# Kernel optimization log

Measured on AMD Instinct MI355X. Metric: run time of the kernel, lower is better.

The kernel has to match this reference:

```python
import jax, jax.numpy as jnp
import numpy as np

NUM_GROUPS = 100
GROUP_SIZE = 100  # uniform group sizes -> total_rows = 10000
TOTAL_ROWS = NUM_GROUPS * GROUP_SIZE
NUM_CLASSES = 1000
BATCH = 4096
EPS = 1e-12


def setup_inputs() -> dict:
    key = jax.random.key(0)
    k1, k2 = jax.random.split(key)
    # one active row per group per sample (multi-hot over groups)
    local_idx = jax.random.randint(k1, (BATCH, NUM_GROUPS), 0, GROUP_SIZE)
    row_idx = local_idx + jnp.arange(NUM_GROUPS) * GROUP_SIZE  # (B, G) global row ids
    x_onehot = jnp.zeros((BATCH, TOTAL_ROWS), dtype=jnp.float32)
    x_onehot = x_onehot.at[jnp.arange(BATCH)[:, None], row_idx].set(1.0)
    # xavier_normal_ on (total_rows, num_classes)
    std = float(np.sqrt(2.0 / (TOTAL_ROWS + NUM_CLASSES)))
    W_logits = jax.random.normal(k2, (TOTAL_ROWS, NUM_CLASSES), dtype=jnp.float32) * std
    bias = jnp.zeros((NUM_CLASSES,), dtype=jnp.float32)
    return {"x_onehot": x_onehot, "W_logits": W_logits, "bias": bias}


def reference(x_onehot, W_logits, bias):
    # per-group softmax over rows (dim=0 within each group), then log(. + eps)
    Wg = W_logits.reshape(NUM_GROUPS, GROUP_SIZE, NUM_CLASSES)
    theta = jax.nn.softmax(Wg, axis=1)
    W = jnp.log(theta + EPS).reshape(TOTAL_ROWS, NUM_CLASSES)
    logits = x_onehot @ W + bias  # (B, C)
    return jax.nn.softmax(logits, axis=-1)
```

## Files before the change

### kernel.cpp

```cpp
#include <hip/hip_runtime.h>
#include <math.h>

#define NUM_GROUPS 100
#define GROUP_SIZE 100
#define TOTAL_ROWS 10000
#define NUM_CLASSES 1000
#define BATCH 4096
#define SPB 16
#define GATHER_BLOCKS (BATCH / SPB)
#define NSLICE 5
#define SLICE_ROWS (GROUP_SIZE / NSLICE)
#define ROW_U 256
#define EXTRACT_BLOCKS 2500
#define PREP_BLOCKS (NUM_GROUPS * NSLICE)

#define QSCALE     (0.08f / 127.0f)
#define QINVSCALE  (127.0f / 0.08f)

__device__ __forceinline__ int q8(float f) {
    int q = __float2int_rn(f * QINVSCALE);
    return max(-127, min(127, q));
}

__global__ __launch_bounds__(256)
void k_stage(const float* __restrict__ W, const float* __restrict__ x,
             float* __restrict__ Sp, unsigned int* __restrict__ Wq,
             int* __restrict__ idxB) {
    const int bid = blockIdx.x;
    const int tid = threadIdx.x;

    if (bid < EXTRACT_BLOCKS) {
        const float4* x4 = (const float4*)x;
        const int base = bid * 4096 + tid;
        #pragma unroll
        for (int k0 = 0; k0 < 16; k0 += 8) {
            float4 v[8];
            #pragma unroll
            for (int u = 0; u < 8; ++u)
                v[u] = x4[base + (k0 + u) * 256];
            #pragma unroll
            for (int u = 0; u < 8; ++u) {
                float4 vv = v[u];
                if (vv.x > 0.5f || vv.y > 0.5f || vv.z > 0.5f || vv.w > 0.5f) {
                    int i  = base + (k0 + u) * 256;
                    int b  = i / 2500;
                    int r4 = i - b * 2500;
                    int g  = r4 / 25;
                    int j  = r4 * 4;
                    int val = vv.x > 0.5f ? j
                            : (vv.y > 0.5f ? j + 1 : (vv.z > 0.5f ? j + 2 : j + 3));
                    idxB[b * NUM_GROUPS + g] = val;
                }
            }
        }
    } else {
        const int pid = bid - EXTRACT_BLOCKS;
        const int g   = pid / NSLICE;
        const int h   = pid % NSLICE;
        const int r0  = h * SLICE_ROWS;

        const float4* Wr = (const float4*)(W + (size_t)(g * GROUP_SIZE + r0) * NUM_CLASSES);
        unsigned int* Wqr = Wq + (size_t)(g * GROUP_SIZE + r0) * ROW_U;

        if (tid < 250) {
            float4 s = make_float4(0.f, 0.f, 0.f, 0.f);
            #pragma unroll
            for (int k0 = 0; k0 < SLICE_ROWS; k0 += 5) {
                float4 v[5];
                #pragma unroll
                for (int u = 0; u < 5; ++u)
                    v[u] = Wr[(size_t)(k0 + u) * 250 + tid];
                #pragma unroll
                for (int u = 0; u < 5; ++u) {
                    float4 vv = v[u];
                    s.x += __expf(vv.x); s.y += __expf(vv.y);
                    s.z += __expf(vv.z); s.w += __expf(vv.w);
                    unsigned int p = (unsigned int)((q8(vv.x) + 128) & 255)
                                   | (((unsigned int)((q8(vv.y) + 128) & 255)) << 8)
                                   | (((unsigned int)((q8(vv.z) + 128) & 255)) << 16)
                                   | (((unsigned int)((q8(vv.w) + 128) & 255)) << 24);
                    Wqr[(size_t)(k0 + u) * ROW_U + tid] = p;
                }
            }
            *(float4*)(Sp + (size_t)(g * NSLICE + h) * NUM_CLASSES + tid * 4) = s;
        }
        if (tid < SLICE_ROWS * 6) {
            int r = tid / 6, p = 250 + tid % 6;
            Wqr[(size_t)r * ROW_U + p] = 0x80808080u;
        }
    }
}

__global__ __launch_bounds__(256)
void k_combine(const float* __restrict__ Sp, const float* __restrict__ bias,
               float* __restrict__ base) {
    __shared__ float part[50][5];
    const int t = threadIdx.x;
    if (t < 250) {
        const int cl = t / 5, p = t % 5;
        const int c  = blockIdx.x * 50 + cl;
        float acc = 0.f;
        #pragma unroll 4
        for (int g = p * 20; g < p * 20 + 20; ++g) {
            const float* q = Sp + (size_t)g * NSLICE * NUM_CLASSES + c;
            float S = q[0];
            #pragma unroll
            for (int h = 1; h < NSLICE; ++h) S += q[h * NUM_CLASSES];
            acc += __logf(S);
        }
        part[cl][p] = acc;
    }
    __syncthreads();
    if (t < 50) {
        const int c = blockIdx.x * 50 + t;
        float s = part[t][0] + part[t][1] + part[t][2] + part[t][3] + part[t][4];
        base[c] = bias[c] - s - 12800.0f * QSCALE;
    }
    if (blockIdx.x == 0 && t < 24) base[NUM_CLASSES + t] = 0.0f;
}

__global__ __launch_bounds__(1024, 1)
void k_gather(const int* __restrict__ idxB, const uint4* __restrict__ Wq4,
              const float* __restrict__ base, float* __restrict__ out) {
    const int tid = threadIdx.x;
    const int w   = tid >> 6;
    const int l   = tid & 63;
    const int b0  = blockIdx.x * SPB;

    const int* myidx = idxB + (size_t)(b0 + w) * NUM_GROUPS;
    const int idxlo = myidx[l];
    const int idxhi = myidx[(l < 36) ? (64 + l) : 63];

    unsigned int acc[8];
    #pragma unroll
    for (int k = 0; k < 8; ++k) acc[k] = 0u;

    uint4 va[4], vb[4];

    auto loadchunk = [&](int ch, uint4 v[4]) {
        #pragma unroll
        for (int u = 0; u < 4; ++u) {
            int gg = ch * 4 + u;
            int r = (gg < 64) ? __builtin_amdgcn_readlane(idxlo, gg)
                              : __builtin_amdgcn_readlane(idxhi, gg - 64);
            v[u] = Wq4[(size_t)r * 64 + l];
        }
    };
    auto consume = [&](uint4 v[4]) {
        #pragma unroll
        for (int u = 0; u < 4; ++u) {
            unsigned int q;
            q = v[u].x; acc[0] += q & 0x00FF00FFu; acc[1] += (q >> 8) & 0x00FF00FFu;
            q = v[u].y; acc[2] += q & 0x00FF00FFu; acc[3] += (q >> 8) & 0x00FF00FFu;
            q = v[u].z; acc[4] += q & 0x00FF00FFu; acc[5] += (q >> 8) & 0x00FF00FFu;
            q = v[u].w; acc[6] += q & 0x00FF00FFu; acc[7] += (q >> 8) & 0x00FF00FFu;
        }
    };

    loadchunk(0, va);
    loadchunk(1, vb);
    for (int c = 0; c < 24; c += 2) {
        __builtin_amdgcn_s_barrier();
        consume(va);
        loadchunk(c + 2, va);
        consume(vb);
        if (c + 3 < 25) loadchunk(c + 3, vb);
    }
    __builtin_amdgcn_s_barrier();
    consume(va);

    float f[16];
    #pragma unroll
    for (int p = 0; p < 4; ++p) {
        unsigned int ae = acc[2 * p], ao = acc[2 * p + 1];
        f[4 * p + 0] = QSCALE * (float)(ae & 0xFFFFu);
        f[4 * p + 1] = QSCALE * (float)(ao & 0xFFFFu);
        f[4 * p + 2] = QSCALE * (float)(ae >> 16);
        f[4 * p + 3] = QSCALE * (float)(ao >> 16);
    }
    const float* bp = base + 16 * l;
    #pragma unroll
    for (int k = 0; k < 16; k += 4) {
        float4 b4 = *(const float4*)(bp + k);
        f[k] += b4.x; f[k + 1] += b4.y; f[k + 2] += b4.z; f[k + 3] += b4.w;
    }

    float m = -INFINITY;
    #pragma unroll
    for (int k = 0; k < 8; ++k) m = fmaxf(m, f[k]);
    if (l < 62) {
        #pragma unroll
        for (int k = 8; k < 16; ++k) m = fmaxf(m, f[k]);
    }
    if (l == 63) m = -INFINITY;
    #pragma unroll
    for (int off = 32; off > 0; off >>= 1)
        m = fmaxf(m, __shfl_xor(m, off, 64));

    float e[16];
    float ls = 0.0f;
    #pragma unroll
    for (int k = 0; k < 16; ++k) e[k] = __expf(f[k] - m);
    #pragma unroll
    for (int k = 0; k < 8; ++k) ls += e[k];
    if (l < 62) {
        #pragma unroll
        for (int k = 8; k < 16; ++k) ls += e[k];
    }
    if (l == 63) ls = 0.0f;
    #pragma unroll
    for (int off = 32; off > 0; off >>= 1)
        ls += __shfl_xor(ls, off, 64);
    const float inv = 1.0f / ls;

    float* op = out + (size_t)(b0 + w) * NUM_CLASSES + 16 * l;
    const int nst = (l < 62) ? 4 : (l == 62 ? 2 : 0);
    #pragma unroll
    for (int s = 0; s < 4; ++s)
        if (s < nst)
            *(float4*)(op + 4 * s) = make_float4(e[4 * s] * inv, e[4 * s + 1] * inv,
                                                 e[4 * s + 2] * inv, e[4 * s + 3] * inv);
}

extern "C" void kernel_launch(void* const* d_in, const int* in_sizes, int n_in,
                              void* d_out, int out_size, void* d_ws, size_t ws_size,
                              hipStream_t stream) {
    const float* x    = (const float*)d_in[0];
    const float* W    = (const float*)d_in[1];
    const float* bias = (const float*)d_in[2];
    float* out = (float*)d_out;

    char* ws = (char*)d_ws;
    float*        base = (float*)ws;
    float*        Sp   = (float*)(ws + 4096);
    unsigned int* Wq   = (unsigned int*)(ws + 4096 + NUM_GROUPS * NSLICE * NUM_CLASSES * 4);
    int*          idxB = (int*)((char*)Wq + (size_t)TOTAL_ROWS * ROW_U * 4);

    k_stage<<<EXTRACT_BLOCKS + PREP_BLOCKS, 256, 0, stream>>>(W, x, Sp, Wq, idxB);
    k_combine<<<20, 256, 0, stream>>>(Sp, bias, base);
    k_gather<<<GATHER_BLOCKS, 1024, 0, stream>>>(idxB, (const uint4*)Wq, base, out);
}
```

Baseline: 299.2 us.

## Fuse combine kernel into stage via last-blocks atomic ticket, use v_perm in gather

Removes the separate k_combine launch. The prep blocks are moved to the front of the grid, and the last 20 prep blocks to arrive, counted with a global atomic ticket, spin-wait until all prep blocks finish and then compute the per-class log-sum base. The gather inner loop replaces a shift-and-mask with a single v_perm byte select. The change adds a memset launch and relies on spin-waiting blocks, which assumes the earlier prep blocks are already resident and can make progress.

```diff
diff --git a/kernel.cpp b/kernel.cpp
--- a/kernel.cpp
+++ b/kernel.cpp
@@ -25,24 +25,25 @@
 __global__ __launch_bounds__(256)
 void k_stage(const float* __restrict__ W, const float* __restrict__ x,
              float* __restrict__ Sp, unsigned int* __restrict__ Wq,
-             int* __restrict__ idxB) {
+             int* __restrict__ idxB, const float* __restrict__ bias,
+             float* __restrict__ base, int* __restrict__ cnt) {
     const int bid = blockIdx.x;
     const int tid = threadIdx.x;
 
-    if (bid < EXTRACT_BLOCKS) {
+    if (bid >= PREP_BLOCKS) {
         const float4* x4 = (const float4*)x;
-        const int base = bid * 4096 + tid;
+        const int bbase = (bid - PREP_BLOCKS) * 4096 + tid;
         #pragma unroll
         for (int k0 = 0; k0 < 16; k0 += 8) {
             float4 v[8];
             #pragma unroll
             for (int u = 0; u < 8; ++u)
-                v[u] = x4[base + (k0 + u) * 256];
+                v[u] = x4[bbase + (k0 + u) * 256];
             #pragma unroll
             for (int u = 0; u < 8; ++u) {
                 float4 vv = v[u];
                 if (vv.x > 0.5f || vv.y > 0.5f || vv.z > 0.5f || vv.w > 0.5f) {
-                    int i  = base + (k0 + u) * 256;
+                    int i  = bbase + (k0 + u) * 256;
                     int b  = i / 2500;
                     int r4 = i - b * 2500;
                     int g  = r4 / 25;
@@ -53,70 +54,86 @@
                 }
             }
         }
-    } else {
-        const int pid = bid - EXTRACT_BLOCKS;
-        const int g   = pid / NSLICE;
-        const int h   = pid % NSLICE;
-        const int r0  = h * SLICE_ROWS;
-
-        const float4* Wr = (const float4*)(W + (size_t)(g * GROUP_SIZE + r0) * NUM_CLASSES);
-        unsigned int* Wqr = Wq + (size_t)(g * GROUP_SIZE + r0) * ROW_U;
-
-        if (tid < 250) {
-            float4 s = make_float4(0.f, 0.f, 0.f, 0.f);
-            #pragma unroll
-            for (int k0 = 0; k0 < SLICE_ROWS; k0 += 5) {
-                float4 v[5];
-                #pragma unroll
-                for (int u = 0; u < 5; ++u)
-                    v[u] = Wr[(size_t)(k0 + u) * 250 + tid];
-                #pragma unroll
-                for (int u = 0; u < 5; ++u) {
-                    float4 vv = v[u];
-                    s.x += __expf(vv.x); s.y += __expf(vv.y);
-                    s.z += __expf(vv.z); s.w += __expf(vv.w);
-                    unsigned int p = (unsigned int)((q8(vv.x) + 128) & 255)
-                                   | (((unsigned int)((q8(vv.y) + 128) & 255)) << 8)
-                                   | (((unsigned int)((q8(vv.z) + 128) & 255)) << 16)
-                                   | (((unsigned int)((q8(vv.w) + 128) & 255)) << 24);
-                    Wqr[(size_t)(k0 + u) * ROW_U + tid] = p;
-                }
+        return;
+    }
+
+    const int pid = bid;
+    const int g   = pid / NSLICE;
+    const int h   = pid % NSLICE;
+    const int r0  = h * SLICE_ROWS;
+
+    const float4* Wr = (const float4*)(W + (size_t)(g * GROUP_SIZE + r0) * NUM_CLASSES);
+    unsigned int* Wqr = Wq + (size_t)(g * GROUP_SIZE + r0) * ROW_U;
+
+    if (tid < 250) {
+        float4 s = make_float4(0.f, 0.f, 0.f, 0.f);
+        #pragma unroll
+        for (int k0 = 0; k0 < SLICE_ROWS; k0 += 5) {
+            float4 v[5];
+            #pragma unroll
+            for (int u = 0; u < 5; ++u)
+                v[u] = Wr[(size_t)(k0 + u) * 250 + tid];
+            #pragma unroll
+            for (int u = 0; u < 5; ++u) {
+                float4 vv = v[u];
+                s.x += __expf(vv.x); s.y += __expf(vv.y);
+                s.z += __expf(vv.z); s.w += __expf(vv.w);
+                unsigned int p = (unsigned int)((q8(vv.x) + 128) & 255)
+                               | (((unsigned int)((q8(vv.y) + 128) & 255)) << 8)
+                               | (((unsigned int)((q8(vv.z) + 128) & 255)) << 16)
+                               | (((unsigned int)((q8(vv.w) + 128) & 255)) << 24);
+                Wqr[(size_t)(k0 + u) * ROW_U + tid] = p;
             }
-            *(float4*)(Sp + (size_t)(g * NSLICE + h) * NUM_CLASSES + tid * 4) = s;
-        }
-        if (tid < SLICE_ROWS * 6) {
-            int r = tid / 6, p = 250 + tid % 6;
-            Wqr[(size_t)r * ROW_U + p] = 0x80808080u;
-        }
-    }
-}
-
-__global__ __launch_bounds__(256)
-void k_combine(const float* __restrict__ Sp, const float* __restrict__ bias,
-               float* __restrict__ base) {
+        }
+        *(float4*)(Sp + (size_t)(g * NSLICE + h) * NUM_CLASSES + tid * 4) = s;
+    }
+    if (tid < SLICE_ROWS * 6) {
+        int r = tid / 6, p = 250 + tid % 6;
+        Wqr[(size_t)r * ROW_U + p] = 0x80808080u;
+    }
+
+    __shared__ int s_ticket;
+    __threadfence();
+    __syncthreads();
+    if (tid == 0) {
+        int t = __hip_atomic_fetch_add(cnt, 1, __ATOMIC_ACQ_REL,
+                                       __HIP_MEMORY_SCOPE_AGENT);
+        s_ticket = t;
+        if (t >= PREP_BLOCKS - 20) {
+            while (__hip_atomic_load(cnt, __ATOMIC_ACQUIRE,
+                                     __HIP_MEMORY_SCOPE_AGENT) < PREP_BLOCKS)
+                __builtin_amdgcn_s_sleep(8);
+        }
+    }
+    __syncthreads();
+    const int ticket = s_ticket;
+    if (ticket < PREP_BLOCKS - 20) return;
+
+    __threadfence();
+    const int cb = ticket - (PREP_BLOCKS - 20);
+
     __shared__ float part[50][5];
-    const int t = threadIdx.x;
-    if (t < 250) {
-        const int cl = t / 5, p = t % 5;
-        const int c  = blockIdx.x * 50 + cl;
+    if (tid < 250) {
+        const int cl = tid / 5, p = tid % 5;
+        const int c  = cb * 50 + cl;
         float acc = 0.f;
         #pragma unroll 4
-        for (int g = p * 20; g < p * 20 + 20; ++g) {
-            const float* q = Sp + (size_t)g * NSLICE * NUM_CLASSES + c;
+        for (int gg = p * 20; gg < p * 20 + 20; ++gg) {
+            const float* q = Sp + (size_t)gg * NSLICE * NUM_CLASSES + c;
             float S = q[0];
             #pragma unroll
-            for (int h = 1; h < NSLICE; ++h) S += q[h * NUM_CLASSES];
+            for (int hh = 1; hh < NSLICE; ++hh) S += q[hh * NUM_CLASSES];
             acc += __logf(S);
         }
         part[cl][p] = acc;
     }
     __syncthreads();
-    if (t < 50) {
-        const int c = blockIdx.x * 50 + t;
-        float s = part[t][0] + part[t][1] + part[t][2] + part[t][3] + part[t][4];
+    if (tid < 50) {
+        const int c = cb * 50 + tid;
+        float s = part[tid][0] + part[tid][1] + part[tid][2] + part[tid][3] + part[tid][4];
         base[c] = bias[c] - s - 12800.0f * QSCALE;
     }
-    if (blockIdx.x == 0 && t < 24) base[NUM_CLASSES + t] = 0.0f;
+    if (cb == 0 && tid < 24) base[NUM_CLASSES + tid] = 0.0f;
 }
 
 __global__ __launch_bounds__(1024, 1)
@@ -150,10 +167,14 @@
         #pragma unroll
         for (int u = 0; u < 4; ++u) {
             unsigned int q;
-            q = v[u].x; acc[0] += q & 0x00FF00FFu; acc[1] += (q >> 8) & 0x00FF00FFu;
-            q = v[u].y; acc[2] += q & 0x00FF00FFu; acc[3] += (q >> 8) & 0x00FF00FFu;
-            q = v[u].z; acc[4] += q & 0x00FF00FFu; acc[5] += (q >> 8) & 0x00FF00FFu;
-            q = v[u].w; acc[6] += q & 0x00FF00FFu; acc[7] += (q >> 8) & 0x00FF00FFu;
+            q = v[u].x; acc[0] += q & 0x00FF00FFu;
+                        acc[1] += __builtin_amdgcn_perm(q, q, 0x0C030C01u);
+            q = v[u].y; acc[2] += q & 0x00FF00FFu;
+                        acc[3] += __builtin_amdgcn_perm(q, q, 0x0C030C01u);
+            q = v[u].z; acc[4] += q & 0x00FF00FFu;
+                        acc[5] += __builtin_amdgcn_perm(q, q, 0x0C030C01u);
+            q = v[u].w; acc[6] += q & 0x00FF00FFu;
+                        acc[7] += __builtin_amdgcn_perm(q, q, 0x0C030C01u);
         }
     };
 
@@ -235,8 +256,10 @@
     float*        Sp   = (float*)(ws + 4096);
     unsigned int* Wq   = (unsigned int*)(ws + 4096 + NUM_GROUPS * NSLICE * NUM_CLASSES * 4);
     int*          idxB = (int*)((char*)Wq + (size_t)TOTAL_ROWS * ROW_U * 4);
-
-    k_stage<<<EXTRACT_BLOCKS + PREP_BLOCKS, 256, 0, stream>>>(W, x, Sp, Wq, idxB);
-    k_combine<<<20, 256, 0, stream>>>(Sp, bias, base);
+    int*          cnt  = (int*)((char*)idxB + (size_t)BATCH * NUM_GROUPS * 4);
+
+    hipMemsetAsync(cnt, 0, 4, stream);
+    k_stage<<<EXTRACT_BLOCKS + PREP_BLOCKS, 256, 0, stream>>>(W, x, Sp, Wq, idxB,
+                                                              bias, base, cnt);
     k_gather<<<GATHER_BLOCKS, 1024, 0, stream>>>(idxB, (const uint4*)Wq, base, out);
 }
```

After: 399.6 us. 33.6% more time.
